# Kernel tuning notes

Measured on AMD Instinct MI355X. Metric: run time of the kernel, lower is better.

The kernel has to match this reference:

```python
import jax, jax.numpy as jnp
import numpy as np

B, FH, N, TIN = 8, 8, 2048, 5      # batch(time for LSTM), f_length, nodes, in_length
H1, H2 = 32, 64                    # traj_linear_hidden, lstm_encoder_size
NEG = -9e15

def setup_inputs() -> dict:
    key = jax.random.key(0)
    ks = jax.random.split(key, 12)
    s = lambda k, shape, fan: jax.random.normal(k, shape, jnp.float32) * (1.0 / np.sqrt(fan))
    return {
        "hist": jax.random.normal(ks[0], (B, FH, N, TIN), jnp.float32),
        "adj": jax.random.randint(ks[1], (B, 2, N, N), 0, 2, jnp.int32),
        "W1": s(ks[2], (H1, TIN * FH), TIN * FH),
        "b1": jnp.zeros((H1,), jnp.float32),
        "W_ih": s(ks[3], (4 * H2, H1), H1),
        "W_hh": s(ks[4], (4 * H2, H2), H2),
        "b_ih": jnp.zeros((4 * H2,), jnp.float32),
        "b_hh": jnp.zeros((4 * H2,), jnp.float32),
        "Wg": s(ks[5], (H2, H2), H2),
        "a_src": s(ks[6], (H2,), H2),
        "a_dst": s(ks[7], (H2,), H2),
    }

def _lstm(x, W_ih, W_hh, b_ih, b_hh):
    # x: [T, Nb, H1] (torch nn.LSTM seq-first); gate order i,f,g,o
    Nb = x.shape[1]
    h0 = jnp.zeros((Nb, H2), x.dtype)
    c0 = jnp.zeros((Nb, H2), x.dtype)
    def step(carry, xt):
        h, c = carry
        g = xt @ W_ih.T + b_ih + h @ W_hh.T + b_hh        # [Nb, 4*H2]
        i, f, gg, o = jnp.split(g, 4, axis=-1)
        c = jax.nn.sigmoid(f) * c + jax.nn.sigmoid(i) * jnp.tanh(gg)
        h = jax.nn.sigmoid(o) * jnp.tanh(c)
        return (h, c), h
    _, hs = jax.lax.scan(step, (h0, c0), x)
    return hs                                              # [T, Nb, H2]

def reference(hist, adj, W1, b1, W_ih, W_hh, b_ih, b_hh, Wg, a_src, a_dst):
    # hist.permute(0,2,3,1).flatten(2,3) -> [B, N, TIN*FH]
    x = jnp.transpose(hist, (0, 2, 3, 1)).reshape(B, N, TIN * FH)
    h1 = jax.nn.elu(x @ W1.T + b1)                         # [B, N, H1]
    hs = _lstm(h1, W_ih, W_hh, b_ih, b_hh)                 # [B, N, H2]
    # GAT over adj[:, -1]
    A = adj[:, -1, :, :] > 0                               # [B, N, N]
    Wh = hs @ Wg                                           # [B, N, H2]
    e = jax.nn.leaky_relu(
        (Wh @ a_src)[:, :, None] + (Wh @ a_dst)[:, None, :], 0.2)
    e = jnp.where(A, e, NEG)
    alpha = jax.nn.softmax(e, axis=-1)                     # [B, N, N]
    out = jax.nn.elu(jnp.einsum("bij,bjd->bid", alpha, Wh))
    return out
```

## Files before the change

### kernel.cpp

```cpp
#include <hip/hip_runtime.h>
#include <hip/hip_bf16.h>
#include <math.h>

#define BB 8
#define FH 8
#define NN 2048
#define TIN 5
#define H1 32
#define H2 64

typedef const void* cvp;
typedef __attribute__((ext_vector_type(8))) short short8;
typedef __attribute__((ext_vector_type(4))) float floatx4;

__device__ __forceinline__ float ldx(cvp p, int i, int bf) {
  if (bf) return __bfloat162float(((const __hip_bfloat16*)p)[i]);
  return ((const float*)p)[i];
}

__device__ __forceinline__ float4 ld4(cvp p, int i, int bf) {
  if (bf) {
    const __hip_bfloat162* q = (const __hip_bfloat162*)p;
    float2 a = __bfloat1622float2(q[(i >> 1)]);
    float2 b = __bfloat1622float2(q[(i >> 1) + 1]);
    return make_float4(a.x, a.y, b.x, b.y);
  }
  return ((const float4*)p)[i >> 2];
}

__device__ __forceinline__ float sigf(float x) {
  return 1.f / (1.f + __expf(-x));
}

__device__ __forceinline__ int detect_bf(cvp wih) {
  unsigned word = ((const unsigned*)wih)[threadIdx.x & 63];
  unsigned e = (word >> 7) & 0xFFu;
  unsigned long long bal = __ballot(e >= 100u && e <= 150u);
  return __popcll(bal) > 44;
}

__global__ __launch_bounds__(256, 2) void k_lstm(
    cvp hist, cvp W1, cvp b1, cvp W_ih, cvp W_hh, cvp b_ih, cvp b_hh,
    float* __restrict__ hs) {
  __shared__ __align__(16) float xh[4][96];
  __shared__ float gbuf[4][256];
  __shared__ float W1s[H1][41];
  __shared__ float b1s[H1];
  __shared__ float xstage[4][40];
  int bf = detect_bf(W_ih);
  int tid = threadIdx.x;
  int w = tid >> 6, lane = tid & 63;
  int g = (w << 6) + lane;
  int n0 = blockIdx.x << 2;
  int node_w = n0 + w;

  for (int i = tid; i < H1 * 40; i += 256) W1s[i / 40][i % 40] = ldx(W1, i, bf);
  if (tid < H1) b1s[tid] = ldx(b1, tid, bf);

  float wreg[96];
#pragma unroll
  for (int kq = 0; kq < 8; ++kq) {
    float4 v = ld4(W_ih, g * 32 + (kq << 2), bf);
    wreg[(kq << 2) + 0] = v.x; wreg[(kq << 2) + 1] = v.y;
    wreg[(kq << 2) + 2] = v.z; wreg[(kq << 2) + 3] = v.w;
  }
#pragma unroll
  for (int kq = 0; kq < 16; ++kq) {
    float4 v = ld4(W_hh, g * 64 + (kq << 2), bf);
    wreg[32 + (kq << 2) + 0] = v.x; wreg[32 + (kq << 2) + 1] = v.y;
    wreg[32 + (kq << 2) + 2] = v.z; wreg[32 + (kq << 2) + 3] = v.w;
  }
  float bias = ldx(b_ih, g, bf) + ldx(b_hh, g, bf);

  xh[w][32 + lane] = 0.f;
  float c = 0.f;

  for (int t = 0; t < BB; ++t) {
    if (tid < 160) {
      int nd = tid / 40, r = tid % 40;
      int ti = r >> 3, f = r & 7;
      xstage[nd][r] = ldx(hist, ((t * FH + f) * NN + n0 + nd) * TIN + ti, bf);
    }
    __syncthreads();
    if (tid < 128) {
      int nd = tid >> 5, k = tid & 31;
      float acc = b1s[k];
#pragma unroll
      for (int j = 0; j < 40; ++j) acc += W1s[k][j] * xstage[nd][j];
      xh[nd][k] = (acc > 0.f) ? acc : expm1f(acc);
    }
    __syncthreads();
    float acc[4] = {bias, bias, bias, bias};
    const float4* xq0 = (const float4*)xh[0];
    const float4* xq1 = (const float4*)xh[1];
    const float4* xq2 = (const float4*)xh[2];
    const float4* xq3 = (const float4*)xh[3];
#pragma unroll
    for (int kq = 0; kq < 24; ++kq) {
      float w0 = wreg[(kq << 2) + 0], w1 = wreg[(kq << 2) + 1];
      float w2 = wreg[(kq << 2) + 2], w3 = wreg[(kq << 2) + 3];
      float4 v0 = xq0[kq], v1 = xq1[kq], v2 = xq2[kq], v3 = xq3[kq];
      acc[0] += w0 * v0.x + w1 * v0.y + w2 * v0.z + w3 * v0.w;
      acc[1] += w0 * v1.x + w1 * v1.y + w2 * v1.z + w3 * v1.w;
      acc[2] += w0 * v2.x + w1 * v2.y + w2 * v2.z + w3 * v2.w;
      acc[3] += w0 * v3.x + w1 * v3.y + w2 * v3.z + w3 * v3.w;
    }
#pragma unroll
    for (int nd = 0; nd < 4; ++nd) gbuf[nd][g] = acc[nd];
    __syncthreads();
    float gi = gbuf[w][lane];
    float gf = gbuf[w][64 + lane];
    float gg = gbuf[w][128 + lane];
    float go = gbuf[w][192 + lane];
    c = sigf(gf) * c + sigf(gi) * tanhf(gg);
    float h = sigf(go) * tanhf(c);
    xh[w][32 + lane] = h;
    hs[((t * NN + node_w) * H2) + lane] = h;
    __syncthreads();
  }
}

__global__ __launch_bounds__(256) void k_gatprep(
    const float* __restrict__ hs, cvp Wg, cvp a_src, cvp a_dst, cvp W_ih,
    __hip_bfloat16* __restrict__ WhFr, float* __restrict__ sv,
    float* __restrict__ dv) {
  __shared__ float wg[H2 * H2];
  __shared__ float tile[32][H2 + 1];
  int bf = detect_bf(W_ih);
  int tid = threadIdx.x;
  for (int i = tid; i < H2 * H2; i += 256) wg[i] = ldx(Wg, i, bf);
  __syncthreads();
  int wave = tid >> 6, lane = tid & 63;
  int b = blockIdx.x >> 6;
  int jt = blockIdx.x & 63;
  int j0 = jt << 5;
  float as = ldx(a_src, lane, bf);
  float ad = ldx(a_dst, lane, bf);
#pragma unroll
  for (int rr = 0; rr < 8; ++rr) {
    int jl = (wave << 3) + rr;
    int row = b * NN + j0 + jl;
    float hreg = hs[row * H2 + lane];
    float acc = 0.f;
#pragma unroll
    for (int k = 0; k < H2; ++k)
      acc += __shfl(hreg, k, 64) * wg[(k << 6) + lane];
    tile[jl][lane] = acc;
    float s = acc * as, d = acc * ad;
#pragma unroll
    for (int off = 32; off > 0; off >>= 1) {
      s += __shfl_xor(s, off, 64);
      d += __shfl_xor(d, off, 64);
    }
    if (lane == 0) { sv[row] = s; dv[row] = d; }
  }
  __syncthreads();
  int nt = tid >> 6, l = tid & 63;
  int q = l >> 4, m = l & 15;
  float v[8];
#pragma unroll
  for (int jj = 0; jj < 8; ++jj)
    v[jj] = tile[(q << 3) + jj][(nt << 4) + m];
  short8 fr;
#pragma unroll
  for (int p = 0; p < 4; ++p)
    ((__hip_bfloat162*)&fr)[p] =
        __float22bfloat162_rn(make_float2(v[2 * p], v[2 * p + 1]));
  size_t off = ((size_t)(b * 64 + jt) * 4 + nt) * 64 + l;
  ((short8*)WhFr)[off] = fr;
}

__global__ __launch_bounds__(256, 4) void k_gat(
    const int* __restrict__ adj, const __hip_bfloat16* __restrict__ WhFr,
    const float* __restrict__ sv, const float* __restrict__ dv,
    void* __restrict__ out, cvp W_ih) {
  __shared__ __align__(16) float dv_s[NN];
  __shared__ unsigned int msk[16 * 65];
  __shared__ floatx4 abuf[3][5][64];
  int bf = detect_bf(W_ih);
  int tid = threadIdx.x;
  int w = tid >> 6, lane = tid & 63;
  int b = blockIdx.x >> 7;
  int i0 = (blockIdx.x & 127) << 4;
  int q = lane >> 4, m = lane & 15;

  for (int j = tid; j < 16 * 65; j += 256) msk[j] = 0u;
  for (int j = tid; j < NN; j += 256) dv_s[j] = dv[b * NN + j];
  float sva = sv[b * NN + i0 + m];
  __syncthreads();

  const int4* adj4 = (const int4*)(adj + ((size_t)(b * 2 + 1) * NN + i0) * NN);
#pragma unroll 16
  for (int gi = 0; gi < 32; ++gi) {
    int g = (w << 5) + gi;
    int row = g >> 3, seg = g & 7;
    int4 v = adj4[(size_t)row * 512 + (seg << 6) + lane];
    unsigned nib = (v.x != 0 ? 1u : 0u) | (v.y != 0 ? 2u : 0u) |
                   (v.z != 0 ? 4u : 0u) | (v.w != 0 ? 8u : 0u);
    atomicOr(&msk[row * 65 + (seg << 3) + (lane >> 3)], nib << ((lane & 7) << 2));
  }
  __syncthreads();

  short8 ones;
#pragma unroll
  for (int p = 0; p < 8; ++p) ones[p] = (short)0x3F80;

  const short8* base = ((const short8*)WhFr) + (size_t)b * 16384 + lane;
  int ksb = w << 4, kse = ksb + 16;
  floatx4 acc0 = {0.f, 0.f, 0.f, 0.f};
  floatx4 acc1 = acc0, acc2 = acc0, acc3 = acc0, accS = acc0;

  for (int ks = ksb; ks < kse; ++ks) {
    const short8* b_ks = base + (size_t)ks * 256;
    short8 b0 = b_ks[0];
    short8 b1 = b_ks[64];
    short8 b2 = b_ks[128];
    short8 b3 = b_ks[192];
    unsigned mword = msk[m * 65 + ks];
    float4 d0 = *(const float4*)&dv_s[(ks << 5) + (q << 3)];
    float4 d1 = *(const float4*)&dv_s[(ks << 5) + (q << 3) + 4];
    float dd[8] = {d0.x, d0.y, d0.z, d0.w, d1.x, d1.y, d1.z, d1.w};
    float pv[8];
#pragma unroll
    for (int jj = 0; jj < 8; ++jj) {
      float t = sva + dd[jj];
      float e = __expf(fmaxf(t, 0.2f * t));
      pv[jj] = ((mword >> ((q << 3) + jj)) & 1u) ? e : 0.f;
    }
    short8 afr;
#pragma unroll
    for (int p2 = 0; p2 < 4; ++p2)
      ((__hip_bfloat162*)&afr)[p2] =
          __float22bfloat162_rn(make_float2(pv[2 * p2], pv[2 * p2 + 1]));
    acc0 = __builtin_amdgcn_mfma_f32_16x16x32_bf16(afr, b0, acc0, 0, 0, 0);
    acc1 = __builtin_amdgcn_mfma_f32_16x16x32_bf16(afr, b1, acc1, 0, 0, 0);
    acc2 = __builtin_amdgcn_mfma_f32_16x16x32_bf16(afr, b2, acc2, 0, 0, 0);
    acc3 = __builtin_amdgcn_mfma_f32_16x16x32_bf16(afr, b3, acc3, 0, 0, 0);
    accS = __builtin_amdgcn_mfma_f32_16x16x32_bf16(afr, ones, accS, 0, 0, 0);
  }
  if (w > 0) {
    abuf[w - 1][0][lane] = acc0;
    abuf[w - 1][1][lane] = acc1;
    abuf[w - 1][2][lane] = acc2;
    abuf[w - 1][3][lane] = acc3;
    abuf[w - 1][4][lane] = accS;
  }
  __syncthreads();
  if (w != 0) return;
#pragma unroll
  for (int ww = 0; ww < 3; ++ww) {
    acc0 += abuf[ww][0][lane];
    acc1 += abuf[ww][1][lane];
    acc2 += abuf[ww][2][lane];
    acc3 += abuf[ww][3][lane];
    accS += abuf[ww][4][lane];
  }
  floatx4 accs[4] = {acc0, acc1, acc2, acc3};
  float inv[4];
#pragma unroll
  for (int r = 0; r < 4; ++r) inv[r] = 1.f / accS[r];
  if (bf) {
    __hip_bfloat16* o = (__hip_bfloat16*)out;
#pragma unroll
    for (int nt = 0; nt < 4; ++nt)
#pragma unroll
      for (int r = 0; r < 4; ++r) {
        float v = accs[nt][r] * inv[r];
        v = (v > 0.f) ? v : expm1f(v);
        int row = i0 + (q << 2) + r;
        o[((size_t)b * NN + row) * H2 + (nt << 4) + m] = __float2bfloat16(v);
      }
  } else {
    float* o = (float*)out;
#pragma unroll
    for (int nt = 0; nt < 4; ++nt)
#pragma unroll
      for (int r = 0; r < 4; ++r) {
        float v = accs[nt][r] * inv[r];
        v = (v > 0.f) ? v : expm1f(v);
        int row = i0 + (q << 2) + r;
        o[((size_t)b * NN + row) * H2 + (nt << 4) + m] = v;
      }
  }
}

extern "C" void kernel_launch(void* const* d_in, const int* in_sizes, int n_in,
                              void* d_out, int out_size, void* d_ws, size_t ws_size,
                              hipStream_t stream) {
  (void)in_sizes; (void)n_in; (void)out_size; (void)ws_size;
  cvp hist  = d_in[0];
  const int* adj = (const int*)d_in[1];
  cvp W1    = d_in[2];
  cvp b1    = d_in[3];
  cvp W_ih  = d_in[4];
  cvp W_hh  = d_in[5];
  cvp b_ih  = d_in[6];
  cvp b_hh  = d_in[7];
  cvp Wg    = d_in[8];
  cvp a_src = d_in[9];
  cvp a_dst = d_in[10];

  float* ws  = (float*)d_ws;
  float* hs  = ws;
  __hip_bfloat16* WhFr = (__hip_bfloat16*)(hs + BB * NN * H2);
  float* sv  = hs + BB * NN * H2 + 524288;
  float* dv  = sv + BB * NN;

  k_lstm<<<512, 256, 0, stream>>>(hist, W1, b1, W_ih, W_hh, b_ih, b_hh, hs);
  k_gatprep<<<512, 256, 0, stream>>>(hs, Wg, a_src, a_dst, W_ih, WhFr, sv, dv);
  k_gat<<<1024, 256, 0, stream>>>(adj, WhFr, sv, dv, d_out, W_ih);
}
```

Measured before the change: 420.3 us.

## Fuse GAT projection and attention-score prep into LSTM kernel epilogue

Removes the separate gatprep kernel: each LSTM step now multiplies the new hidden state by Wg held in registers, reduces the src/dst attention scores with wave shuffles, and writes the bf16 fragment layout directly. This drops the fp32 hs round trip to global memory and one kernel launch. In exchange it adds 64 more registers per thread in a kernel already holding 96 weight registers under launch_bounds(256,2), which risks spills or lower occupancy, and it replaces the coalesced short8 fragment stores with scattered 2-byte stores.

```diff
diff --git a/kernel.cpp b/kernel.cpp
--- a/kernel.cpp
+++ b/kernel.cpp
@@ -41,7 +41,9 @@
 
 __global__ __launch_bounds__(256, 2) void k_lstm(
     cvp hist, cvp W1, cvp b1, cvp W_ih, cvp W_hh, cvp b_ih, cvp b_hh,
-    float* __restrict__ hs) {
+    cvp Wg, cvp a_src, cvp a_dst,
+    __hip_bfloat16* __restrict__ WhFr, float* __restrict__ sv,
+    float* __restrict__ dv) {
   __shared__ __align__(16) float xh[4][96];
   __shared__ float gbuf[4][256];
   __shared__ float W1s[H1][41];
@@ -50,7 +52,7 @@
   int bf = detect_bf(W_ih);
   int tid = threadIdx.x;
   int w = tid >> 6, lane = tid & 63;
-  int g = (w << 6) + lane;
+  int g = tid;
   int n0 = blockIdx.x << 2;
   int node_w = n0 + w;
 
@@ -71,6 +73,16 @@
     wreg[32 + (kq << 2) + 2] = v.z; wreg[32 + (kq << 2) + 3] = v.w;
   }
   float bias = ldx(b_ih, g, bf) + ldx(b_hh, g, bf);
+
+  float wgreg[64];
+#pragma unroll
+  for (int k = 0; k < H2; ++k) wgreg[k] = ldx(Wg, (k << 6) + lane, bf);
+  float as = ldx(a_src, lane, bf);
+  float ad = ldx(a_dst, lane, bf);
+
+  size_t o8base = ((size_t)(node_w >> 5) * 256) + ((size_t)(lane >> 4) * 64) +
+                  (((node_w >> 3) & 3) * 16) + (lane & 15);
+  int jj = node_w & 7;
 
   xh[w][32 + lane] = 0.f;
   float c = 0.f;
@@ -115,59 +127,28 @@
     c = sigf(gf) * c + sigf(gi) * tanhf(gg);
     float h = sigf(go) * tanhf(c);
     xh[w][32 + lane] = h;
-    hs[((t * NN + node_w) * H2) + lane] = h;
-    __syncthreads();
-  }
-}
-
-__global__ __launch_bounds__(256) void k_gatprep(
-    const float* __restrict__ hs, cvp Wg, cvp a_src, cvp a_dst, cvp W_ih,
-    __hip_bfloat16* __restrict__ WhFr, float* __restrict__ sv,
-    float* __restrict__ dv) {
-  __shared__ float wg[H2 * H2];
-  __shared__ float tile[32][H2 + 1];
-  int bf = detect_bf(W_ih);
-  int tid = threadIdx.x;
-  for (int i = tid; i < H2 * H2; i += 256) wg[i] = ldx(Wg, i, bf);
-  __syncthreads();
-  int wave = tid >> 6, lane = tid & 63;
-  int b = blockIdx.x >> 6;
-  int jt = blockIdx.x & 63;
-  int j0 = jt << 5;
-  float as = ldx(a_src, lane, bf);
-  float ad = ldx(a_dst, lane, bf);
-#pragma unroll
-  for (int rr = 0; rr < 8; ++rr) {
-    int jl = (wave << 3) + rr;
-    int row = b * NN + j0 + jl;
-    float hreg = hs[row * H2 + lane];
-    float acc = 0.f;
-#pragma unroll
-    for (int k = 0; k < H2; ++k)
-      acc += __shfl(hreg, k, 64) * wg[(k << 6) + lane];
-    tile[jl][lane] = acc;
-    float s = acc * as, d = acc * ad;
+
+    float wh = 0.f;
+    const float4* hq = (const float4*)&xh[w][32];
+#pragma unroll
+    for (int kq = 0; kq < 16; ++kq) {
+      float4 hv = hq[kq];
+      wh += hv.x * wgreg[(kq << 2) + 0] + hv.y * wgreg[(kq << 2) + 1] +
+            hv.z * wgreg[(kq << 2) + 2] + hv.w * wgreg[(kq << 2) + 3];
+    }
+    float s = wh * as, d = wh * ad;
 #pragma unroll
     for (int off = 32; off > 0; off >>= 1) {
       s += __shfl_xor(s, off, 64);
       d += __shfl_xor(d, off, 64);
     }
-    if (lane == 0) { sv[row] = s; dv[row] = d; }
-  }
-  __syncthreads();
-  int nt = tid >> 6, l = tid & 63;
-  int q = l >> 4, m = l & 15;
-  float v[8];
-#pragma unroll
-  for (int jj = 0; jj < 8; ++jj)
-    v[jj] = tile[(q << 3) + jj][(nt << 4) + m];
-  short8 fr;
-#pragma unroll
-  for (int p = 0; p < 4; ++p)
-    ((__hip_bfloat162*)&fr)[p] =
-        __float22bfloat162_rn(make_float2(v[2 * p], v[2 * p + 1]));
-  size_t off = ((size_t)(b * 64 + jt) * 4 + nt) * 64 + l;
-  ((short8*)WhFr)[off] = fr;
+    if (lane == 0) {
+      sv[t * NN + node_w] = s;
+      dv[t * NN + node_w] = d;
+    }
+    WhFr[((size_t)t * 16384 + o8base) * 8 + jj] = __float2bfloat16(wh);
+    __syncthreads();
+  }
 }
 
 __global__ __launch_bounds__(256, 4) void k_gat(
@@ -300,13 +281,11 @@
   cvp a_src = d_in[9];
   cvp a_dst = d_in[10];
 
-  float* ws  = (float*)d_ws;
-  float* hs  = ws;
-  __hip_bfloat16* WhFr = (__hip_bfloat16*)(hs + BB * NN * H2);
-  float* sv  = hs + BB * NN * H2 + 524288;
-  float* dv  = sv + BB * NN;
-
-  k_lstm<<<512, 256, 0, stream>>>(hist, W1, b1, W_ih, W_hh, b_ih, b_hh, hs);
-  k_gatprep<<<512, 256, 0, stream>>>(hs, Wg, a_src, a_dst, W_ih, WhFr, sv, dv);
+  __hip_bfloat16* WhFr = (__hip_bfloat16*)d_ws;
+  float* sv = (float*)d_ws + 524288;
+  float* dv = sv + BB * NN;
+
+  k_lstm<<<512, 256, 0, stream>>>(hist, W1, b1, W_ih, W_hh, b_ih, b_hh,
+                                  Wg, a_src, a_dst, WhFr, sv, dv);
   k_gat<<<1024, 256, 0, stream>>>(adj, WhFr, sv, dv, d_out, W_ih);
 }
```

Result: faster. 398.4 us (-5.2%).
